# Kernel tuning notes

Hardware: AMD Instinct MI355X
Metric: run time of the kernel (lower is better)

The kernel has to match this reference:

```python
import jax, jax.numpy as jnp
import numpy as np
import math

D_IN, D_MODEL, N_HEADS, N_LAYERS, D_FF = 128, 256, 4, 4, 1024
NUM_BANDS = D_MODEL // 6  # 42 -> 252 encoding dims, zero-padded to 256
LN_EPS = 1e-5


def setup_inputs() -> dict:
    key = jax.random.key(0)
    ks = jax.random.split(key, 32)
    N, B = 65536, 128
    s = 0.02
    L, D, F = N_LAYERS, D_MODEL, D_FF
    inp = {
        "dom_embeddings": jax.random.normal(ks[0], (N, D_IN), jnp.float32),
        "dom_to_event_idx": jnp.sort(jax.random.randint(ks[1], (N,), 0, B)),
        "batch_size": B,
        "geometry": jax.random.normal(ks[2], (N, 3), jnp.float32),
        "in_proj_w": jax.random.normal(ks[3], (D, D_IN), jnp.float32) * s,
        "in_proj_b": jnp.zeros((D,), jnp.float32),
        "geo_proj_w": jax.random.normal(ks[4], (D, D), jnp.float32) * s,
        "geo_proj_b": jnp.zeros((D,), jnp.float32),
        "cls_token": jax.random.normal(ks[5], (1, 1, D), jnp.float32),
        "qkv_w": jax.random.normal(ks[6], (L, 3 * D, D), jnp.float32) * s,
        "qkv_b": jnp.zeros((L, 3 * D), jnp.float32),
        "out_w": jax.random.normal(ks[7], (L, D, D), jnp.float32) * s,
        "out_b": jnp.zeros((L, D), jnp.float32),
        "ln1_w": jnp.ones((L, D), jnp.float32),
        "ln1_b": jnp.zeros((L, D), jnp.float32),
        "ln2_w": jnp.ones((L, D), jnp.float32),
        "ln2_b": jnp.zeros((L, D), jnp.float32),
        "ff_w1": jax.random.normal(ks[8], (L, F, D), jnp.float32) * s,
        "ff_b1": jnp.zeros((L, F), jnp.float32),
        "ff_w2": jax.random.normal(ks[9], (L, D, F), jnp.float32) * s,
        "ff_b2": jnp.zeros((L, D), jnp.float32),
        "head_w1": jax.random.normal(ks[10], (D, D), jnp.float32) * s,
        "head_b1": jnp.zeros((D,), jnp.float32),
        "head_w2": jax.random.normal(ks[11], (2, D), jnp.float32) * s,
        "head_b2": jnp.zeros((2,), jnp.float32),
    }
    return inp


def _layer_norm(x, w, b):
    m = x.mean(-1, keepdims=True)
    v = ((x - m) ** 2).mean(-1, keepdims=True)
    return (x - m) / jnp.sqrt(v + LN_EPS) * w + b


def _pos_enc(geometry):
    # geometry: (N,3). Order: per coord -> per freq -> [sin, cos]; pad to D_MODEL.
    freqs = jnp.logspace(0.0, 1.0, NUM_BANDS, dtype=jnp.float32)  # 1..max_freq=10
    ang = 2.0 * math.pi * geometry[:, :, None] * freqs[None, None, :]  # (N,3,F)
    sc = jnp.stack([jnp.sin(ang), jnp.cos(ang)], axis=-1)  # (N,3,F,2)
    enc = sc.reshape(geometry.shape[0], 3 * NUM_BANDS * 2)  # (N,252)
    pad = D_MODEL - enc.shape[1]
    return jnp.pad(enc, ((0, 0), (0, pad)))


def _self_attn(x, pad_mask, Wqkv, bqkv, Wo, bo):
    B, S, D = x.shape
    H, hd = N_HEADS, D // N_HEADS
    qkv = x @ Wqkv.T + bqkv  # (B,S,3D)
    q, k, v = jnp.split(qkv, 3, axis=-1)
    q = q.reshape(B, S, H, hd).transpose(0, 2, 1, 3)
    k = k.reshape(B, S, H, hd).transpose(0, 2, 1, 3)
    v = v.reshape(B, S, H, hd).transpose(0, 2, 1, 3)
    scores = jnp.einsum('bhqd,bhkd->bhqk', q, k) / math.sqrt(hd)
    scores = jnp.where(pad_mask[:, None, None, :], -jnp.inf, scores)
    a = jax.nn.softmax(scores, axis=-1)
    o = jnp.einsum('bhqk,bhkd->bhqd', a, v).transpose(0, 2, 1, 3).reshape(B, S, D)
    return o @ Wo.T + bo


def reference(dom_embeddings, dom_to_event_idx, batch_size, geometry,
              in_proj_w, in_proj_b, geo_proj_w, geo_proj_b, cls_token,
              qkv_w, qkv_b, out_w, out_b, ln1_w, ln1_b, ln2_w, ln2_b,
              ff_w1, ff_b1, ff_w2, ff_b2, head_w1, head_b1, head_w2, head_b2):
    N = dom_embeddings.shape[0]
    B = int(batch_size)
    x = dom_embeddings @ in_proj_w.T + in_proj_b  # (N,D)
    geo = _pos_enc(geometry) @ geo_proj_w.T + geo_proj_b
    x = x + geo

    # Vectorized scatter-pack (replaces per-DOM Python loop).
    counts = jnp.bincount(dom_to_event_idx, length=B)
    starts = jnp.concatenate([jnp.zeros((1,), counts.dtype), jnp.cumsum(counts)[:-1]])
    pos = jnp.arange(N) - starts[dom_to_event_idx] + 1  # slot 0 reserved for CLS
    max_doms = int(counts.max())
    S = max_doms + 1

    batch_tensor = jnp.zeros((B, S, D_MODEL), x.dtype)
    batch_tensor = batch_tensor.at[:, 0, :].set(cls_token[0, 0])
    batch_tensor = batch_tensor.at[dom_to_event_idx, pos].set(x)
    # True = padded. NOTE: CLS slot stays True, faithful to original code.
    pad_mask = jnp.ones((B, S), bool).at[dom_to_event_idx, pos].set(False)

    h = batch_tensor
    for l in range(N_LAYERS):  # pre-LN encoder layers
        h = h + _self_attn(_layer_norm(h, ln1_w[l], ln1_b[l]), pad_mask,
                           qkv_w[l], qkv_b[l], out_w[l], out_b[l])
        ff_in = _layer_norm(h, ln2_w[l], ln2_b[l])
        h = h + jax.nn.relu(ff_in @ ff_w1[l].T + ff_b1[l]) @ ff_w2[l].T + ff_b2[l]

    cls = h[:, 0, :]
    hid = jax.nn.relu(cls @ head_w1.T + head_b1)
    return hid @ head_w2.T + head_b2  # (B,2)
```

## Files before the change

kernel.cpp:

```cpp
#include <hip/hip_runtime.h>
#include <hip/hip_bf16.h>
#include <math.h>


#define D_INPUT  128
#define DM       256
#define NHEADS   4
#define HDIM     64
#define NLAYERS  4
#define DFF      1024
#define BEV      128
#define LNEPS    1e-5f
#define KT       10
#define SCL      0.18033688011112042f

typedef unsigned short u16;
typedef __attribute__((ext_vector_type(8))) short bf16x8;
typedef __attribute__((ext_vector_type(4))) float f32x4;

__device__ inline u16 f2bf(float x) {
    unsigned int xi = __float_as_uint(x);
    unsigned int r  = xi + 0x7FFFu + ((xi >> 16) & 1u);
    return (u16)(r >> 16);
}
__device__ inline unsigned int cvtpk(float lo, float hi) {
    unsigned int r;
    asm("v_cvt_pk_bf16_f32 %0, %1, %2" : "=v"(r) : "v"(lo), "v"(hi));
    return r;
}

__device__ inline void gload16(const void* g, void* l) {
    __builtin_amdgcn_global_load_lds(
        (const __attribute__((address_space(1))) unsigned int*)g,
        (__attribute__((address_space(3))) unsigned int*)l, 16, 0, 0);
}


__global__ void starts_kernel(const int* __restrict__ idx, int* __restrict__ counts,
                              int* __restrict__ starts, int N) {
    __shared__ int bnd[BEV + 1];
    const int b = threadIdx.x;
    if (b <= BEV) {
        int lo = 0, hi = N;
        while (lo < hi) { int mid = (lo + hi) >> 1; if (idx[mid] < b) lo = mid + 1; else hi = mid; }
        bnd[b] = lo;
    }
    __syncthreads();
    if (b < BEV) { starts[b] = bnd[b]; counts[b] = bnd[b + 1] - bnd[b]; }
}

__global__ void r2bs_kernel(const int* __restrict__ idx, const int* __restrict__ starts,
                            int* __restrict__ r2bs, int N, int TP) {
    int i = blockIdx.x * blockDim.x + threadIdx.x;
    if (i < N) {
        int b = idx[i];
        r2bs[i] = (b << 16) | (i - starts[b] + 1);
    } else if (i < N + BEV) {
        r2bs[i] = (i - N) << 16;
    } else if (i < TP) {
        r2bs[i] = BEV << 16;
    }
}

__global__ void beacon_kernel(float* out, int n, float v) {
    int i = blockIdx.x * blockDim.x + threadIdx.x;
    if (i < n) out[i] = v;
}

__global__ void cvt4_kernel(const float* __restrict__ s0, const float* __restrict__ s1,
                            const float* __restrict__ s2, const float* __restrict__ s3,
                            u16* __restrict__ d0, u16* __restrict__ d1,
                            u16* __restrict__ d2, u16* __restrict__ d3,
                            int n0, int n1, int n2, int n3) {
    int i = blockIdx.x * blockDim.x + threadIdx.x;
    if (i < n0) { d0[i] = f2bf(s0[i]); return; }
    i -= n0;
    if (i < n1) { d1[i] = f2bf(s1[i]); return; }
    i -= n1;
    if (i < n2) { d2[i] = f2bf(s2[i]); return; }
    i -= n2;
    if (i < n3) d3[i] = f2bf(s3[i]);
}

__global__ void prep_w_kernel(const float* __restrict__ win, const float* __restrict__ wgeo,
                              const float* __restrict__ bin, const float* __restrict__ bgeo,
                              u16* __restrict__ We, float* __restrict__ be) {
    int i = blockIdx.x * blockDim.x + threadIdx.x;
    if (i < 256 * 384) {
        int o = i / 384, k = i % 384;
        float v = 0.f;
        if (k < 128)      v = win[o * 128 + k];
        else if (k < 380) v = wgeo[o * 256 + (k - 128)];
        We[i] = f2bf(v);
    }
    if (i < 256) be[i] = bin[i] + bgeo[i];
}

__global__ void prep_a_kernel(const float* __restrict__ emb, const float* __restrict__ geo,
                              u16* __restrict__ A, int N) {
    size_t i = (size_t)blockIdx.x * blockDim.x + threadIdx.x;
    if (i >= (size_t)N * 384) return;
    int k = (int)(i % 384);
    size_t r = i / 384;
    float v = 0.f;
    if (k < 128) {
        v = emb[r * 128 + k];
    } else if (k < 380) {
        int rem  = k - 128;
        int axis = rem / 84;
        int r2   = rem % 84;
        int band = r2 >> 1;
        int sc   = r2 & 1;
        float freq = expf((float)band * (2.3025850929940457f / 41.0f));
        float ang  = (6.283185307179586f * geo[r * 3 + axis]) * freq;
        v = sc ? cosf(ang) : sinf(ang);
    }
    A[i] = f2bf(v);
}

__global__ void cls_kernel(const float* __restrict__ cls, float* __restrict__ h, int N) {
    h[(size_t)(N + blockIdx.x) * DM + threadIdx.x] = cls[threadIdx.x];
}


__global__ __launch_bounds__(256) void ln_kernel(const float* __restrict__ x,
                                                 const float* __restrict__ w,
                                                 const float* __restrict__ b,
                                                 u16* __restrict__ y, int T) {
    int row  = blockIdx.x * 4 + (threadIdx.x >> 6);
    int lane = threadIdx.x & 63;
    if (row >= T) return;
    float4 v = ((const float4*)(x + (size_t)row * DM))[lane];
    float s = v.x + v.y + v.z + v.w;
    #pragma unroll
    for (int off = 32; off > 0; off >>= 1) s += __shfl_xor(s, off);
    float mean = s * (1.0f / 256.0f);
    float dx = v.x - mean, dy = v.y - mean, dz = v.z - mean, dw = v.w - mean;
    float ss = dx * dx + dy * dy + dz * dz + dw * dw;
    #pragma unroll
    for (int off = 32; off > 0; off >>= 1) ss += __shfl_xor(ss, off);
    float inv = rsqrtf(ss * (1.0f / 256.0f) + LNEPS);
    float4 wv = ((const float4*)w)[lane];
    float4 bv = ((const float4*)b)[lane];
    ushort4 o;
    o.x = f2bf(dx * inv * wv.x + bv.x);
    o.y = f2bf(dy * inv * wv.y + bv.y);
    o.z = f2bf(dz * inv * wv.z + bv.z);
    o.w = f2bf(dw * inv * wv.w + bv.w);
    ((ushort4*)(y + (size_t)row * DM))[lane] = o;
}


template <typename OutT>
__global__ __launch_bounds__(512) void mgemm_kernel(const u16* __restrict__ A,
                                                    const u16* __restrict__ W,
                                                    const float* __restrict__ bias,
                                                    OutT* __restrict__ C,
                                                    int K, int No, int ldc, int flags,
                                                    const int* __restrict__ r2bs,
                                                    u16* __restrict__ KVt) {
    __shared__ u16 As[256 * 64];
    __shared__ u16 Bs[128 * 64];
    const int m0 = blockIdx.y * 256, n0 = blockIdx.x * 128;
    const int tid  = threadIdx.x;
    const int w    = tid >> 6, lane = tid & 63;
    const int wr   = w >> 1,  wc   = w & 1;
    const int lhi  = lane >> 4, llo = lane & 15;

    f32x4 acc[4][4];
    #pragma unroll
    for (int i = 0; i < 4; ++i)
        #pragma unroll
        for (int j = 0; j < 4; ++j) acc[i][j] = (f32x4){0.f, 0.f, 0.f, 0.f};

    for (int kt = 0; kt < K; kt += 64) {
        __syncthreads();
        #pragma unroll
        for (int it = 0; it < 4; ++it) {
            int un = it * 512 + tid;
            int r = un >> 3, c8 = un & 7;
            gload16(A + (size_t)(m0 + r) * K + kt + ((c8 ^ (r & 7)) * 8), &As[un * 8]);
        }
        #pragma unroll
        for (int it = 0; it < 2; ++it) {
            int un = it * 512 + tid;
            int r = un >> 3, c8 = un & 7;
            gload16(W + (size_t)(n0 + r) * K + kt + ((c8 ^ (r & 7)) * 8), &Bs[un * 8]);
        }
        __syncthreads();
        #pragma unroll
        for (int kk = 0; kk < 2; ++kk) {
            bf16x8 af[4], bfr[4];
            #pragma unroll
            for (int i = 0; i < 4; ++i) {
                const int row = wr * 64 + i * 16 + llo;
                af[i] = *(const bf16x8*)&As[row * 64 + (((kk * 4 + lhi) ^ (row & 7)) * 8)];
            }
            #pragma unroll
            for (int j = 0; j < 4; ++j) {
                const int row = wc * 64 + j * 16 + llo;
                bfr[j] = *(const bf16x8*)&Bs[row * 64 + (((kk * 4 + lhi) ^ (row & 7)) * 8)];
            }
            #pragma unroll
            for (int i = 0; i < 4; ++i)
                #pragma unroll
                for (int j = 0; j < 4; ++j)
                    acc[i][j] = __builtin_amdgcn_mfma_f32_16x16x32_bf16(af[i], bfr[j], acc[i][j], 0, 0, 0);
        }
    }

    const int vmode = (flags & 4) ? (n0 >= 512 ? 2 : (n0 >= 256 ? 1 : 0)) : 0;
    #pragma unroll
    for (int i = 0; i < 4; ++i) {
        const int row0 = m0 + wr * 64 + i * 16 + lhi * 4;
        int bsr[4];
        if (vmode) {
            #pragma unroll
            for (int r = 0; r < 4; ++r) bsr[r] = r2bs[row0 + r];
        }
        #pragma unroll
        for (int j = 0; j < 4; ++j) {
            const int col = n0 + wc * 64 + j * 16 + llo;
            const float bb = bias[col];
            if (vmode == 1) {
                const int hh = (col - 256) >> 6, d = (col - 256) & 63;
                const int kk_t = d >> 5, lhi_t = (d >> 3) & 3, e = d & 7;
                #pragma unroll
                for (int r = 0; r < 4; ++r) {
                    const int eb = bsr[r] >> 16, pos = bsr[r] & 0xffff;
                    const int ktile = pos >> 6;
                    if (ktile < KT) {
                        const int unit = ((pos & 63) >> 4) * 2 + kk_t;
                        const int lane_t = lhi_t * 16 + (pos & 15);
                        KVt[(((size_t)(eb * 4 + hh) * 2 + 0) * KT + ktile) * 4096
                            + unit * 512 + lane_t * 8 + e] = f2bf(acc[i][j][r] + bb);
                    }
                }
            } else if (vmode == 2) {
                const int hh = (col - 512) >> 6, d = (col - 512) & 63;
                const int i_t = d >> 4, llo_t = d & 15;
                #pragma unroll
                for (int r = 0; r < 4; ++r) {
                    const int eb = bsr[r] >> 16, pos = bsr[r] & 0xffff;
                    const int ktile = pos >> 6;
                    if (ktile < KT) {
                        const int unit = i_t * 2 + ((pos & 63) >> 5);
                        const int lane_t = (((pos & 63) >> 3) & 3) * 16 + llo_t;
                        KVt[(((size_t)(eb * 4 + hh) * 2 + 1) * KT + ktile) * 4096
                            + unit * 512 + lane_t * 8 + (pos & 7)] = f2bf(acc[i][j][r] + bb);
                    }
                }
            } else {
                #pragma unroll
                for (int r = 0; r < 4; ++r) {
                    float v = acc[i][j][r] + bb;
                    if ((flags & 8) && col < 256) v *= SCL;
                    size_t idx = (size_t)(row0 + r) * ldc + col;
                    if constexpr (sizeof(OutT) == 4) {
                        float* cp = (float*)C + idx;
                        if (flags & 2) v += *cp;
                        if (flags & 1) v = fmaxf(v, 0.f);
                        *cp = v;
                    } else {
                        if (flags & 1) v = fmaxf(v, 0.f);
                        ((u16*)C)[idx] = f2bf(v);
                    }
                }
            }
        }
    }
}


__global__ __launch_bounds__(512) void mgemmln_kernel(const u16* __restrict__ X,
                                                      const u16* __restrict__ W,
                                                      const float* __restrict__ bias,
                                                      float* __restrict__ H,
                                                      const float* __restrict__ lnw,
                                                      const float* __restrict__ lnb,
                                                      u16* __restrict__ Y,
                                                      int K) {
    __shared__ u16 Xs[128 * 64];
    __shared__ u16 Ws[256 * 64];
    __shared__ float part[2][4][128];
    const int m0 = blockIdx.y * 128;
    const int tid = threadIdx.x;
    const int w = tid >> 6, lane = tid & 63;
    const int wr = w >> 2, wc = w & 3;
    const int lhi = lane >> 4, llo = lane & 15;

    f32x4 acc[4][4];
    #pragma unroll
    for (int i = 0; i < 4; ++i)
        #pragma unroll
        for (int j = 0; j < 4; ++j) acc[i][j] = (f32x4){0.f, 0.f, 0.f, 0.f};

    for (int kt = 0; kt < K; kt += 64) {
        __syncthreads();
        #pragma unroll
        for (int it = 0; it < 2; ++it) {
            int un = it * 512 + tid;
            int r = un >> 3, c8 = un & 7;
            gload16(X + (size_t)(m0 + r) * K + kt + ((c8 ^ (r & 7)) * 8), &Xs[un * 8]);
        }
        #pragma unroll
        for (int it = 0; it < 4; ++it) {
            int un = it * 512 + tid;
            int r = un >> 3, c8 = un & 7;
            gload16(W + (size_t)r * K + kt + ((c8 ^ (r & 7)) * 8), &Ws[un * 8]);
        }
        __syncthreads();
        #pragma unroll
        for (int kk = 0; kk < 2; ++kk) {
            bf16x8 xf[4], wf[4];
            #pragma unroll
            for (int i = 0; i < 4; ++i) {
                const int row = wr * 64 + i * 16 + llo;
                xf[i] = *(const bf16x8*)&Xs[row * 64 + (((kk * 4 + lhi) ^ (row & 7)) * 8)];
            }
            #pragma unroll
            for (int j = 0; j < 4; ++j) {
                const int row = wc * 64 + j * 16 + llo;
                wf[j] = *(const bf16x8*)&Ws[row * 64 + (((kk * 4 + lhi) ^ (row & 7)) * 8)];
            }
            #pragma unroll
            for (int i = 0; i < 4; ++i)
                #pragma unroll
                for (int j = 0; j < 4; ++j)
                    acc[i][j] = __builtin_amdgcn_mfma_f32_16x16x32_bf16(wf[j], xf[i], acc[i][j], 0, 0, 0);
        }
    }

    float rsum[4], rsq[4];
    #pragma unroll
    for (int i = 0; i < 4; ++i) { rsum[i] = 0.f; rsq[i] = 0.f; }
    #pragma unroll
    for (int i = 0; i < 4; ++i) {
        const int row = m0 + wr * 64 + i * 16 + llo;
        #pragma unroll
        for (int j = 0; j < 4; ++j) {
            const int col0 = wc * 64 + j * 16 + lhi * 4;
            const float4 bb = *(const float4*)&bias[col0];
            const float4 hv = *(const float4*)&H[(size_t)row * DM + col0];
            float v0 = acc[i][j][0] + bb.x + hv.x;
            float v1 = acc[i][j][1] + bb.y + hv.y;
            float v2 = acc[i][j][2] + bb.z + hv.z;
            float v3 = acc[i][j][3] + bb.w + hv.w;
            acc[i][j][0] = v0; acc[i][j][1] = v1; acc[i][j][2] = v2; acc[i][j][3] = v3;
            rsum[i] += (v0 + v1) + (v2 + v3);
            rsq[i]  += (v0 * v0 + v1 * v1) + (v2 * v2 + v3 * v3);
        }
    }
    #pragma unroll
    for (int i = 0; i < 4; ++i) {
        rsum[i] += __shfl_xor(rsum[i], 16);  rsum[i] += __shfl_xor(rsum[i], 32);
        rsq[i]  += __shfl_xor(rsq[i], 16);   rsq[i]  += __shfl_xor(rsq[i], 32);
    }
    __syncthreads();
    if (lhi == 0) {
        #pragma unroll
        for (int i = 0; i < 4; ++i) {
            const int rl = wr * 64 + i * 16 + llo;
            part[0][wc][rl] = rsum[i];
            part[1][wc][rl] = rsq[i];
        }
    }
    __syncthreads();

    #pragma unroll
    for (int i = 0; i < 4; ++i) {
        const int rl = wr * 64 + i * 16 + llo;
        const int row = m0 + rl;
        const float s = (part[0][0][rl] + part[0][1][rl]) + (part[0][2][rl] + part[0][3][rl]);
        const float q = (part[1][0][rl] + part[1][1][rl]) + (part[1][2][rl] + part[1][3][rl]);
        const float mean = s * (1.0f / 256.0f);
        const float var  = fmaxf(q * (1.0f / 256.0f) - mean * mean, 0.f);
        const float rstd = rsqrtf(var + LNEPS);
        #pragma unroll
        for (int j = 0; j < 4; ++j) {
            const int col0 = wc * 64 + j * 16 + lhi * 4;
            const float4 wv = *(const float4*)&lnw[col0];
            const float4 bv = *(const float4*)&lnb[col0];
            float4 hv;
            hv.x = acc[i][j][0]; hv.y = acc[i][j][1];
            hv.z = acc[i][j][2]; hv.w = acc[i][j][3];
            *(float4*)&H[(size_t)row * DM + col0] = hv;
            uint2 yy;
            yy.x = cvtpk((hv.x - mean) * rstd * wv.x + bv.x,
                         (hv.y - mean) * rstd * wv.y + bv.y);
            yy.y = cvtpk((hv.z - mean) * rstd * wv.z + bv.z,
                         (hv.w - mean) * rstd * wv.w + bv.w);
            *(uint2*)&Y[(size_t)row * DM + col0] = yy;
        }
    }
}


__global__ __launch_bounds__(256) void mattn_kernel(const u16* __restrict__ Qb,
                                                    const u16* __restrict__ KVt,
                                                    const int* __restrict__ counts,
                                                    const int* __restrict__ starts,
                                                    u16* __restrict__ out, int N) {
    const int id  = blockIdx.x;
    const int rem = id >> 3;
    const int qt  = rem % KT;
    const int bh  = (rem / KT) * 8 + (id & 7);
    const int b = bh >> 2, hh = bh & 3;
    const int Sb = counts[b] + 1;
    const int qbase = qt * 64;
    if (qbase >= Sb) return;
    const int start = starts[b];
    __shared__ u16 Pl[4][16 * 72];
    const int tid = threadIdx.x;
    const int w = tid >> 6, lane = tid & 63;
    const int llo = lane & 15, lhi = lane >> 4;

    const int qi = qbase + w * 16 + llo;
    const size_t qrow = (qi < Sb && qi > 0) ? (size_t)(start + qi - 1) : (size_t)(N + b);
    bf16x8 bq[2];
    bq[0] = *(const bf16x8*)(Qb + qrow * 256 + hh * 64 + lhi * 8);
    bq[1] = *(const bf16x8*)(Qb + qrow * 256 + hh * 64 + 32 + lhi * 8);

    const u16* kb = KVt + ((size_t)bh * 2 + 0) * KT * 4096;
    const u16* vb = KVt + ((size_t)bh * 2 + 1) * KT * 4096;

    f32x4 acc[4];
    #pragma unroll
    for (int i = 0; i < 4; ++i) acc[i] = (f32x4){0.f, 0.f, 0.f, 0.f};
    float m = -1e30f, l = 0.f;

    int nt = (Sb + 63) >> 6;
    if (nt > KT) nt = KT;

    for (int t = 0; t < nt; ++t) {
        const int kbase = t * 64;
        const u16* kp = kb + t * 4096 + lane * 8;
        const u16* vp = vb + t * 4096 + lane * 8;

        bf16x8 ak[4][2], av[4][2];
        #pragma unroll
        for (int i = 0; i < 4; ++i) {
            #pragma unroll
            for (int kk = 0; kk < 2; ++kk) {
                ak[i][kk] = *(const bf16x8*)(kp + (i * 2 + kk) * 512);
                av[i][kk] = *(const bf16x8*)(vp + (i * 2 + kk) * 512);
            }
        }

        f32x4 sc[4];
        #pragma unroll
        for (int i = 0; i < 4; ++i) sc[i] = (f32x4){0.f, 0.f, 0.f, 0.f};
        #pragma unroll
        for (int kk = 0; kk < 2; ++kk)
            #pragma unroll
            for (int i = 0; i < 4; ++i)
                sc[i] = __builtin_amdgcn_mfma_f32_16x16x32_bf16(ak[i][kk], bq[kk], sc[i], 0, 0, 0);

        float rm;
        if (kbase + 64 <= Sb) {
            float m0v = fmaxf(fmaxf(sc[0][0], sc[0][1]), fmaxf(sc[0][2], sc[0][3]));
            float m1v = fmaxf(fmaxf(sc[1][0], sc[1][1]), fmaxf(sc[1][2], sc[1][3]));
            float m2v = fmaxf(fmaxf(sc[2][0], sc[2][1]), fmaxf(sc[2][2], sc[2][3]));
            float m3v = fmaxf(fmaxf(sc[3][0], sc[3][1]), fmaxf(sc[3][2], sc[3][3]));
            rm = fmaxf(fmaxf(m0v, m1v), fmaxf(m2v, m3v));
        } else {
            rm = -1e30f;
            #pragma unroll
            for (int i = 0; i < 4; ++i)
                #pragma unroll
                for (int r = 0; r < 4; ++r) {
                    const int key = kbase + i * 16 + lhi * 4 + r;
                    const float s = (key < Sb) ? sc[i][r] : -1e30f;
                    sc[i][r] = s;
                    rm = fmaxf(rm, s);
                }
        }
        rm = fmaxf(rm, __shfl_xor(rm, 16));
        rm = fmaxf(rm, __shfl_xor(rm, 32));

        if (!__all(rm <= m + 8.f)) {
            const float mnew = fmaxf(m, rm);
            const float corr = exp2f(m - mnew);
            l *= corr;
            #pragma unroll
            for (int i = 0; i < 4; ++i) acc[i] *= corr;
            m = mnew;
        }

        float ls = 0.f;
        #pragma unroll
        for (int i = 0; i < 4; ++i) {
            const float p0 = exp2f(sc[i][0] - m), p1 = exp2f(sc[i][1] - m);
            const float p2 = exp2f(sc[i][2] - m), p3 = exp2f(sc[i][3] - m);
            ls += (p0 + p1) + (p2 + p3);
            uint2 pp;
            pp.x = cvtpk(p0, p1);
            pp.y = cvtpk(p2, p3);
            *(uint2*)&Pl[w][llo * 72 + i * 16 + lhi * 4] = pp;
        }
        ls += __shfl_xor(ls, 16);
        ls += __shfl_xor(ls, 32);
        l += ls;

        #pragma unroll
        for (int kk = 0; kk < 2; ++kk) {
            bf16x8 pb = *(const bf16x8*)&Pl[w][llo * 72 + kk * 32 + lhi * 8];
            #pragma unroll
            for (int i = 0; i < 4; ++i)
                acc[i] = __builtin_amdgcn_mfma_f32_16x16x32_bf16(av[i][kk], pb, acc[i], 0, 0, 0);
        }
    }

    if (qi < Sb) {
        const size_t orow = (qi == 0) ? (size_t)(N + b) : (size_t)(start + qi - 1);
        const float invl = 1.f / l;
        #pragma unroll
        for (int i = 0; i < 4; ++i) {
            ushort4 o;
            o.x = f2bf(acc[i][0] * invl);
            o.y = f2bf(acc[i][1] * invl);
            o.z = f2bf(acc[i][2] * invl);
            o.w = f2bf(acc[i][3] * invl);
            *(ushort4*)&out[orow * DM + hh * HDIM + i * 16 + lhi * 4] = o;
        }
    }
}


__global__ __launch_bounds__(256) void head_kernel(const float* __restrict__ h,
                                                   const float* __restrict__ w1,
                                                   const float* __restrict__ b1,
                                                   const float* __restrict__ w2,
                                                   const float* __restrict__ b2,
                                                   float* __restrict__ out, int N) {
    const int b = blockIdx.x;
    const int t = threadIdx.x;
    __shared__ float cls[DM];
    __shared__ float hid[DM];
    cls[t] = h[(size_t)(N + b) * DM + t];
    __syncthreads();
    float s = b1[t];
    for (int k = 0; k < DM; ++k) s = fmaf(cls[k], w1[t * DM + k], s);
    hid[t] = fmaxf(s, 0.f);
    __syncthreads();
    if (t < 2) {
        float o = b2[t];
        for (int k = 0; k < DM; ++k) o = fmaf(hid[k], w2[t * DM + k], o);
        out[b * 2 + t] = o;
    }
}


extern "C" void kernel_launch(void* const* d_in, const int* in_sizes, int n_in,
                              void* d_out, int out_size, void* d_ws, size_t ws_size,
                              hipStream_t stream) {
    const float* dom_emb   = (const float*)d_in[0];
    const int*   dom_idx   = (const int*)d_in[1];
    const float* geometry  = (const float*)d_in[3];
    const float* in_w      = (const float*)d_in[4];
    const float* in_b      = (const float*)d_in[5];
    const float* geo_w     = (const float*)d_in[6];
    const float* geo_b     = (const float*)d_in[7];
    const float* cls_tok   = (const float*)d_in[8];
    const float* qkv_w     = (const float*)d_in[9];
    const float* qkv_b     = (const float*)d_in[10];
    const float* out_w     = (const float*)d_in[11];
    const float* out_b     = (const float*)d_in[12];
    const float* ln1_w     = (const float*)d_in[13];
    const float* ln1_b     = (const float*)d_in[14];
    const float* ln2_w     = (const float*)d_in[15];
    const float* ln2_b     = (const float*)d_in[16];
    const float* ff_w1     = (const float*)d_in[17];
    const float* ff_b1     = (const float*)d_in[18];
    const float* ff_w2     = (const float*)d_in[19];
    const float* ff_b2     = (const float*)d_in[20];
    const float* head_w1   = (const float*)d_in[21];
    const float* head_b1   = (const float*)d_in[22];
    const float* head_w2   = (const float*)d_in[23];
    const float* head_b2   = (const float*)d_in[24];
    float* outp = (float*)d_out;

    const int N  = in_sizes[0] / D_INPUT;
    const int T  = N + BEV;
    const int TP = ((T + 255) / 256) * 256;

    char* base = (char*)d_ws;
    size_t off = 0;
    int* counts = (int*)(base + off);          off += 1024;
    int* starts = (int*)(base + off);          off += 1024;
    u16*   Web  = (u16*)(base + off);          off += (size_t)256 * 384 * 2;
    float* be   = (float*)(base + off);        off += 1024;
    u16*   wq   = (u16*)(base + off);          off += (size_t)NLAYERS * 768 * 256 * 2;
    u16*   wo   = (u16*)(base + off);          off += (size_t)NLAYERS * 256 * 256 * 2;
    u16*   w1b  = (u16*)(base + off);          off += (size_t)NLAYERS * 1024 * 256 * 2;
    u16*   w2b  = (u16*)(base + off);          off += (size_t)NLAYERS * 256 * 1024 * 2;
    int*   r2bs = (int*)(base + off);          off += ((size_t)TP * 4 + 255) & ~255ULL;
    float* h    = (float*)(base + off);        off += (size_t)TP * DM * 4;
    u16*   xb   = (u16*)(base + off);          off += (size_t)TP * DM * 2;
    const size_t qb_sz  = (size_t)TP * 256 * 2;
    const size_t kvt_sz = (size_t)(BEV + 1) * 4 * 2 * KT * 4096 * 2;
    const size_t big2   = qb_sz + kvt_sz;
    const size_t ff1_sz = (size_t)TP * 1024 * 2;
    char* bigc = base + off;
    const bool ff_single = ws_size >= off + (ff1_sz > big2 ? ff1_sz : big2);
    off += ff_single ? (ff1_sz > big2 ? ff1_sz : big2) : big2;

    u16* Ab   = (u16*)bigc;
    u16* Qbuf = (u16*)bigc;
    u16* KVt  = (u16*)(bigc + qb_sz);
    u16* ffm  = (u16*)bigc;

    if (ws_size < off) {
        beacon_kernel<<<1, 256, 0, stream>>>(outp, out_size, (float)(ws_size >> 20));
        return;
    }

    {
        const int n0 = NLAYERS * 768 * 256, n1 = NLAYERS * 256 * 256;
        const int n2 = NLAYERS * 1024 * 256, n3 = NLAYERS * 256 * 1024;
        cvt4_kernel<<<(n0 + n1 + n2 + n3 + 255) / 256, 256, 0, stream>>>(
            qkv_w, out_w, ff_w1, ff_w2, wq, wo, w1b, w2b, n0, n1, n2, n3);
    }
    prep_w_kernel<<<(256 * 384 + 255) / 256, 256, 0, stream>>>(in_w, geo_w, in_b, geo_b, Web, be);

    starts_kernel<<<1, 256, 0, stream>>>(dom_idx, counts, starts, N);
    r2bs_kernel<<<(TP + 255) / 256, 256, 0, stream>>>(dom_idx, starts, r2bs, N, TP);

    prep_a_kernel<<<(int)(((size_t)N * 384 + 255) / 256), 256, 0, stream>>>(dom_emb, geometry, Ab, N);
    mgemm_kernel<float><<<dim3(2, N / 256), 512, 0, stream>>>(
        Ab, Web, be, h, 384, DM, DM, 0, nullptr, nullptr);
    cls_kernel<<<BEV, DM, 0, stream>>>(cls_tok, h, N);

    const int MT = TP / 256;
    const int MT2 = TP / 128;
    int chs[2], nch;
    if (ff_single) { chs[0] = MT; nch = 1; }
    else           { chs[0] = (MT + 1) / 2; chs[1] = MT - chs[0]; nch = 2; }
    ln_kernel<<<TP / 4, 256, 0, stream>>>(h, ln1_w, ln1_b, xb, TP);
    for (int l = 0; l < NLAYERS; ++l) {
        mgemm_kernel<u16><<<dim3(6, MT), 512, 0, stream>>>(
            xb, wq + (size_t)l * 768 * 256, qkv_b + l * 768, Qbuf, 256, 768, 256, 4 | 8,
            r2bs, KVt);
        mattn_kernel<<<8 * KT * (BEV * NHEADS / 8), 256, 0, stream>>>(
            Qbuf, KVt, counts, starts, xb, N);
        mgemmln_kernel<<<dim3(1, MT2), 512, 0, stream>>>(
            xb, wo + (size_t)l * 256 * 256, out_b + l * DM, h,
            ln2_w + l * DM, ln2_b + l * DM, xb, 256);
        const int lnx = (l + 1 < NLAYERS) ? (l + 1) : l;
        int t0 = 0;
        for (int c = 0; c < nch; ++c) {
            const size_t r0 = (size_t)t0 * 256;
            mgemm_kernel<u16><<<dim3(8, chs[c]), 512, 0, stream>>>(
                xb + r0 * DM, w1b + (size_t)l * DFF * 256, ff_b1 + l * DFF, ffm,
                256, DFF, DFF, 1, nullptr, nullptr);
            mgemmln_kernel<<<dim3(1, chs[c] * 2), 512, 0, stream>>>(
                ffm, w2b + (size_t)l * 256 * DFF, ff_b2 + l * DM, h + r0 * DM,
                ln1_w + lnx * DM, ln1_b + lnx * DM, xb + r0 * DM, DFF);
            t0 += chs[c];
        }
    }

    head_kernel<<<BEV, DM, 0, stream>>>(h, head_w1, head_b1, head_w2, head_b2, outp, N);
}
```

Measured before the change: 1.844 ms.

## Pre-pack weights in MFMA fragment order and read them directly from global memory

```diff
diff --git a/kernel.cpp b/kernel.cpp
--- a/kernel.cpp
+++ b/kernel.cpp
@@ -28,11 +28,17 @@
     asm("v_cvt_pk_bf16_f32 %0, %1, %2" : "=v"(r) : "v"(lo), "v"(hi));
     return r;
 }
-
 __device__ inline void gload16(const void* g, void* l) {
     __builtin_amdgcn_global_load_lds(
         (const __attribute__((address_space(1))) unsigned int*)g,
         (__attribute__((address_space(3))) unsigned int*)l, 16, 0, 0);
+}
+
+__device__ inline size_t wpack_off(int col, int k, int nkt) {
+    const int c16 = col >> 4, llo = col & 15;
+    const int kt = k >> 6, kr = k & 63;
+    const int kk = kr >> 5, lhi = (kr >> 3) & 3, e = kr & 7;
+    return ((size_t)(c16 * nkt + kt)) * 1024 + kk * 512 + (lhi * 16 + llo) * 8 + e;
 }
 
 
@@ -67,19 +73,39 @@
     if (i < n) out[i] = v;
 }
 
-__global__ void cvt4_kernel(const float* __restrict__ s0, const float* __restrict__ s1,
-                            const float* __restrict__ s2, const float* __restrict__ s3,
-                            u16* __restrict__ d0, u16* __restrict__ d1,
-                            u16* __restrict__ d2, u16* __restrict__ d3,
-                            int n0, int n1, int n2, int n3) {
+__global__ void cvt4p_kernel(const float* __restrict__ s0, const float* __restrict__ s1,
+                             const float* __restrict__ s2, const float* __restrict__ s3,
+                             u16* __restrict__ d0, u16* __restrict__ d1,
+                             u16* __restrict__ d2, u16* __restrict__ d3) {
+    const int n0 = NLAYERS * 768 * 256, n1 = NLAYERS * 256 * 256;
+    const int n2 = NLAYERS * 1024 * 256, n3 = NLAYERS * 256 * 1024;
     int i = blockIdx.x * blockDim.x + threadIdx.x;
-    if (i < n0) { d0[i] = f2bf(s0[i]); return; }
+    if (i < n0) {
+        const int NoK = 768 * 256;
+        int l = i / NoK, rem = i - l * NoK, col = rem >> 8, k = rem & 255;
+        d0[(size_t)l * NoK + wpack_off(col, k, 4)] = f2bf(s0[i]);
+        return;
+    }
     i -= n0;
-    if (i < n1) { d1[i] = f2bf(s1[i]); return; }
+    if (i < n1) {
+        const int NoK = 256 * 256;
+        int l = i / NoK, rem = i - l * NoK, col = rem >> 8, k = rem & 255;
+        d1[(size_t)l * NoK + wpack_off(col, k, 4)] = f2bf(s1[i]);
+        return;
+    }
     i -= n1;
-    if (i < n2) { d2[i] = f2bf(s2[i]); return; }
+    if (i < n2) {
+        const int NoK = 1024 * 256;
+        int l = i / NoK, rem = i - l * NoK, col = rem >> 8, k = rem & 255;
+        d2[(size_t)l * NoK + wpack_off(col, k, 4)] = f2bf(s2[i]);
+        return;
+    }
     i -= n2;
-    if (i < n3) d3[i] = f2bf(s3[i]);
+    if (i < n3) {
+        const int NoK = 256 * 1024;
+        int l = i / NoK, rem = i - l * NoK, col = rem >> 10, k = rem & 1023;
+        d3[(size_t)l * NoK + wpack_off(col, k, 16)] = f2bf(s3[i]);
+    }
 }
 
 __global__ void prep_w_kernel(const float* __restrict__ win, const float* __restrict__ wgeo,
@@ -91,7 +117,7 @@
         float v = 0.f;
         if (k < 128)      v = win[o * 128 + k];
         else if (k < 380) v = wgeo[o * 256 + (k - 128)];
-        We[i] = f2bf(v);
+        We[wpack_off(o, k, 6)] = f2bf(v);
     }
     if (i < 256) be[i] = bin[i] + bgeo[i];
 }
@@ -153,19 +179,19 @@
 
 template <typename OutT>
 __global__ __launch_bounds__(512) void mgemm_kernel(const u16* __restrict__ A,
-                                                    const u16* __restrict__ W,
+                                                    const u16* __restrict__ Wp,
                                                     const float* __restrict__ bias,
                                                     OutT* __restrict__ C,
                                                     int K, int No, int ldc, int flags,
                                                     const int* __restrict__ r2bs,
                                                     u16* __restrict__ KVt) {
     __shared__ u16 As[256 * 64];
-    __shared__ u16 Bs[128 * 64];
     const int m0 = blockIdx.y * 256, n0 = blockIdx.x * 128;
     const int tid  = threadIdx.x;
     const int w    = tid >> 6, lane = tid & 63;
     const int wr   = w >> 1,  wc   = w & 1;
     const int lhi  = lane >> 4, llo = lane & 15;
+    const int nkt  = K >> 6;
 
     f32x4 acc[4][4];
     #pragma unroll
@@ -181,13 +207,8 @@
             int r = un >> 3, c8 = un & 7;
             gload16(A + (size_t)(m0 + r) * K + kt + ((c8 ^ (r & 7)) * 8), &As[un * 8]);
         }
-        #pragma unroll
-        for (int it = 0; it < 2; ++it) {
-            int un = it * 512 + tid;
-            int r = un >> 3, c8 = un & 7;
-            gload16(W + (size_t)(n0 + r) * K + kt + ((c8 ^ (r & 7)) * 8), &Bs[un * 8]);
-        }
         __syncthreads();
+        const u16* wb = Wp + ((size_t)(kt >> 6)) * 1024 + lane * 8;
         #pragma unroll
         for (int kk = 0; kk < 2; ++kk) {
             bf16x8 af[4], bfr[4];
@@ -198,8 +219,8 @@
             }
             #pragma unroll
             for (int j = 0; j < 4; ++j) {
-                const int row = wc * 64 + j * 16 + llo;
-                bfr[j] = *(const bf16x8*)&Bs[row * 64 + (((kk * 4 + lhi) ^ (row & 7)) * 8)];
+                const int c16 = (n0 >> 4) + wc * 4 + j;
+                bfr[j] = *(const bf16x8*)(wb + ((size_t)c16 * nkt) * 1024 + kk * 512);
             }
             #pragma unroll
             for (int i = 0; i < 4; ++i)
@@ -272,22 +293,21 @@
 }
 
 
-__global__ __launch_bounds__(512) void mgemmln_kernel(const u16* __restrict__ X,
-                                                      const u16* __restrict__ W,
+__global__ __launch_bounds__(256) void mgemmln_kernel(const u16* __restrict__ X,
+                                                      const u16* __restrict__ Wp,
                                                       const float* __restrict__ bias,
                                                       float* __restrict__ H,
                                                       const float* __restrict__ lnw,
                                                       const float* __restrict__ lnb,
                                                       u16* __restrict__ Y,
                                                       int K) {
-    __shared__ u16 Xs[128 * 64];
-    __shared__ u16 Ws[256 * 64];
-    __shared__ float part[2][4][128];
-    const int m0 = blockIdx.y * 128;
+    __shared__ u16 Xs[64 * 64];
+    __shared__ float part[2][4][64];
+    const int m0 = blockIdx.x * 64;
     const int tid = threadIdx.x;
-    const int w = tid >> 6, lane = tid & 63;
-    const int wr = w >> 2, wc = w & 3;
+    const int wc = tid >> 6, lane = tid & 63;
     const int lhi = lane >> 4, llo = lane & 15;
+    const int nkt = K >> 6;
 
     f32x4 acc[4][4];
     #pragma unroll
@@ -299,29 +319,24 @@
         __syncthreads();
         #pragma unroll
         for (int it = 0; it < 2; ++it) {
-            int un = it * 512 + tid;
+            int un = it * 256 + tid;
             int r = un >> 3, c8 = un & 7;
             gload16(X + (size_t)(m0 + r) * K + kt + ((c8 ^ (r & 7)) * 8), &Xs[un * 8]);
         }
-        #pragma unroll
-        for (int it = 0; it < 4; ++it) {
-            int un = it * 512 + tid;
-            int r = un >> 3, c8 = un & 7;
-            gload16(W + (size_t)r * K + kt + ((c8 ^ (r & 7)) * 8), &Ws[un * 8]);
-        }
         __syncthreads();
+        const u16* wb = Wp + ((size_t)(kt >> 6)) * 1024 + lane * 8;
         #pragma unroll
         for (int kk = 0; kk < 2; ++kk) {
             bf16x8 xf[4], wf[4];
             #pragma unroll
             for (int i = 0; i < 4; ++i) {
-                const int row = wr * 64 + i * 16 + llo;
+                const int row = i * 16 + llo;
                 xf[i] = *(const bf16x8*)&Xs[row * 64 + (((kk * 4 + lhi) ^ (row & 7)) * 8)];
             }
             #pragma unroll
             for (int j = 0; j < 4; ++j) {
-                const int row = wc * 64 + j * 16 + llo;
-                wf[j] = *(const bf16x8*)&Ws[row * 64 + (((kk * 4 + lhi) ^ (row & 7)) * 8)];
+                const int c16 = wc * 4 + j;
+                wf[j] = *(const bf16x8*)(wb + ((size_t)c16 * nkt) * 1024 + kk * 512);
             }
             #pragma unroll
             for (int i = 0; i < 4; ++i)
@@ -336,7 +351,7 @@
     for (int i = 0; i < 4; ++i) { rsum[i] = 0.f; rsq[i] = 0.f; }
     #pragma unroll
     for (int i = 0; i < 4; ++i) {
-        const int row = m0 + wr * 64 + i * 16 + llo;
+        const int row = m0 + i * 16 + llo;
         #pragma unroll
         for (int j = 0; j < 4; ++j) {
             const int col0 = wc * 64 + j * 16 + lhi * 4;
@@ -360,7 +375,7 @@
     if (lhi == 0) {
         #pragma unroll
         for (int i = 0; i < 4; ++i) {
-            const int rl = wr * 64 + i * 16 + llo;
+            const int rl = i * 16 + llo;
             part[0][wc][rl] = rsum[i];
             part[1][wc][rl] = rsq[i];
         }
@@ -369,7 +384,7 @@
 
     #pragma unroll
     for (int i = 0; i < 4; ++i) {
-        const int rl = wr * 64 + i * 16 + llo;
+        const int rl = i * 16 + llo;
         const int row = m0 + rl;
         const float s = (part[0][0][rl] + part[0][1][rl]) + (part[0][2][rl] + part[0][3][rl]);
         const float q = (part[1][0][rl] + part[1][1][rl]) + (part[1][2][rl] + part[1][3][rl]);
@@ -616,10 +631,9 @@
     }
 
     {
-        const int n0 = NLAYERS * 768 * 256, n1 = NLAYERS * 256 * 256;
-        const int n2 = NLAYERS * 1024 * 256, n3 = NLAYERS * 256 * 1024;
-        cvt4_kernel<<<(n0 + n1 + n2 + n3 + 255) / 256, 256, 0, stream>>>(
-            qkv_w, out_w, ff_w1, ff_w2, wq, wo, w1b, w2b, n0, n1, n2, n3);
+        const int ntot = NLAYERS * (768 * 256 + 256 * 256 + 1024 * 256 + 256 * 1024);
+        cvt4p_kernel<<<(ntot + 255) / 256, 256, 0, stream>>>(
+            qkv_w, out_w, ff_w1, ff_w2, wq, wo, w1b, w2b);
     }
     prep_w_kernel<<<(256 * 384 + 255) / 256, 256, 0, stream>>>(in_w, geo_w, in_b, geo_b, Web, be);
 
@@ -632,7 +646,6 @@
     cls_kernel<<<BEV, DM, 0, stream>>>(cls_tok, h, N);
 
     const int MT = TP / 256;
-    const int MT2 = TP / 128;
     int chs[2], nch;
     if (ff_single) { chs[0] = MT; nch = 1; }
     else           { chs[0] = (MT + 1) / 2; chs[1] = MT - chs[0]; nch = 2; }
@@ -643,7 +656,7 @@
             r2bs, KVt);
         mattn_kernel<<<8 * KT * (BEV * NHEADS / 8), 256, 0, stream>>>(
             Qbuf, KVt, counts, starts, xb, N);
-        mgemmln_kernel<<<dim3(1, MT2), 512, 0, stream>>>(
+        mgemmln_kernel<<<TP / 64, 256, 0, stream>>>(
             xb, wo + (size_t)l * 256 * 256, out_b + l * DM, h,
             ln2_w + l * DM, ln2_b + l * DM, xb, 256);
         const int lnx = (l + 1 < NLAYERS) ? (l + 1) : l;
@@ -653,7 +666,7 @@
             mgemm_kernel<u16><<<dim3(8, chs[c]), 512, 0, stream>>>(
                 xb + r0 * DM, w1b + (size_t)l * DFF * 256, ff_b1 + l * DFF, ffm,
                 256, DFF, DFF, 1, nullptr, nullptr);
-            mgemmln_kernel<<<dim3(1, chs[c] * 2), 512, 0, stream>>>(
+            mgemmln_kernel<<<chs[c] * 4, 256, 0, stream>>>(
                 ffm, w2b + (size_t)l * 256 * DFF, ff_b2 + l * DM, h + r0 * DM,
                 ln1_w + lnx * DM, ln1_b + lnx * DM, xb + r0 * DM, DFF);
             t0 += chs[c];
```

Result: faster. 1.762 ms (-4.5%).
